# Performance work log

Hardware: AMD Instinct MI355X
Metric: run time of the kernel (lower is better)

The kernel has to match this reference:

```python
import jax, jax.numpy as jnp
import numpy as np
import math

D_MODEL = 1024
D_INNER = 2048
D_HALF = D_INNER // 2
D_STATE = 16
D_CONV = 4
DT_RANK = 64
B_SZ = 4
L = 2048


def _dw_conv(x, w, b):
    # x: (b, l, c), w: (k, 1, c) depthwise, SAME padding
    y = jax.lax.conv_general_dilated(
        x, w, window_strides=(1,), padding='SAME',
        feature_group_count=x.shape[-1],
        dimension_numbers=('NWC', 'WIO', 'NWC'))
    return y + b


def _selective_scan(u, delta, A, Bc, Cc, D):
    # u, delta: (b, l, d); Bc, Cc: (b, l, n); A: (d, n); D: (d,)
    b, l, d = u.shape
    n = A.shape[1]

    def step(h, inp):
        d_t, u_t, B_t, C_t = inp  # (b,d), (b,d), (b,n), (b,n)
        dA = jnp.exp(d_t[..., None] * A)                     # (b,d,n)
        h = dA * h + (d_t * u_t)[..., None] * B_t[:, None, :]
        y = jnp.einsum('bdn,bn->bd', h, C_t)
        return h, y

    h0 = jnp.zeros((b, d, n), u.dtype)
    xs = (jnp.moveaxis(delta, 1, 0), jnp.moveaxis(u, 1, 0),
          jnp.moveaxis(Bc, 1, 0), jnp.moveaxis(Cc, 1, 0))
    _, ys = jax.lax.scan(step, h0, xs)                       # (l,b,d)
    return jnp.moveaxis(ys, 0, 1) + u * D


def setup_inputs() -> dict:
    key = jax.random.key(0)
    ks = jax.random.split(key, 12)
    x = jax.random.normal(ks[0], (B_SZ, L, D_MODEL), jnp.float32)
    W_in = jax.random.normal(ks[1], (D_MODEL, D_INNER), jnp.float32) * (D_MODEL ** -0.5)
    conv_x_w = jax.random.normal(ks[2], (D_CONV, 1, D_HALF), jnp.float32) * (D_CONV ** -0.5)
    conv_x_b = jnp.zeros((D_HALF,), jnp.float32)
    conv_z_w = jax.random.normal(ks[3], (D_CONV, 1, D_HALF), jnp.float32) * (D_CONV ** -0.5)
    conv_z_b = jnp.zeros((D_HALF,), jnp.float32)
    W_xdbl = jax.random.normal(ks[4], (D_HALF, DT_RANK + 2 * D_STATE), jnp.float32) * (D_HALF ** -0.5)
    dt_init_std = DT_RANK ** -0.5  # dt_scale = 1.0
    W_dt = jax.random.uniform(ks[5], (DT_RANK, D_HALF), jnp.float32, -dt_init_std, dt_init_std)
    rand_vals = jax.random.uniform(ks[6], (D_HALF,))
    dt_bias = jnp.exp(rand_vals * (math.log(0.1) - math.log(0.001)) + math.log(0.001))
    dt_bias = jnp.clip(dt_bias, 1e-4)
    inv_dt = dt_bias + jnp.log(-jnp.expm1(-dt_bias))
    D = jnp.ones((D_HALF,), jnp.float32)
    W_out = jax.random.normal(ks[7], (D_INNER, D_MODEL), jnp.float32) * (D_INNER ** -0.5)
    b_out = jnp.zeros((D_MODEL,), jnp.float32)
    return dict(x=x, W_in=W_in, conv_x_w=conv_x_w, conv_x_b=conv_x_b,
                conv_z_w=conv_z_w, conv_z_b=conv_z_b, W_xdbl=W_xdbl,
                W_dt=W_dt, inv_dt=inv_dt, D=D, W_out=W_out, b_out=b_out)


def reference(x, W_in, conv_x_w, conv_x_b, conv_z_w, conv_z_b, W_xdbl,
              W_dt, inv_dt, D, W_out, b_out):
    xz = x @ W_in                                            # (b,l,d_inner), no bias
    xs, z = jnp.split(xz, 2, axis=-1)                        # (b,l,d_half) each
    # A = -exp(log(arange(1..N))) tiled over channels
    A = -jnp.tile(jnp.arange(1, D_STATE + 1, dtype=jnp.float32), (D_HALF, 1))  # (d,n)
    xs = jax.nn.silu(_dw_conv(xs, conv_x_w, conv_x_b))
    z = jax.nn.silu(_dw_conv(z, conv_z_w, conv_z_b))
    x_dbl = xs @ W_xdbl                                      # (b,l,dt_rank+2n)
    dt_low, Bc, Cc = jnp.split(x_dbl, [DT_RANK, DT_RANK + D_STATE], axis=-1)
    dt = dt_low @ W_dt + inv_dt                              # Dense with bias_init=inv_dt
    delta = jax.nn.softplus(dt + inv_dt)                     # scan adds delta_bias=inv_dt again (faithful)
    y = _selective_scan(xs, delta, A, Bc, Cc, D)             # (b,l,d_half)
    y = jnp.concatenate([y, z], axis=-1)                     # (b,l,d_inner)
    return y @ W_out + b_out
```

## Files before the change

kernel.cpp:

```cpp
#include <hip/hip_runtime.h>
#include <hip/hip_bf16.h>
#include <math.h>

#define B_SZ 4
#define LSEQ 2048
#define DM 1024
#define DI 2048
#define DH 1024
#define DS 16
#define DTR 64
#define RTOT 96
#define MROWS (B_SZ * LSEQ)

#define NCH 32
#define CHUNK 64

#define KD 192
#define KDP 200

typedef short bf8_t __attribute__((ext_vector_type(8)));
typedef float f4_t __attribute__((ext_vector_type(4)));

__device__ __forceinline__ unsigned short f2bfbits(float v) {
  __hip_bfloat16 h = __float2bfloat16(v);
  return *(unsigned short*)&h;
}
__device__ __forceinline__ float bfu_lo(unsigned int v) {
  unsigned int x = v << 16;
  return *(float*)&x;
}
__device__ __forceinline__ float bfu_hi(unsigned int v) {
  unsigned int x = v & 0xffff0000u;
  return *(float*)&x;
}
__device__ __forceinline__ float bf16f(unsigned short h) {
  unsigned int x = ((unsigned int)h) << 16;
  return *(float*)&x;
}

__device__ __forceinline__ void gl_lds16(const void* g, void* l) {
  __builtin_amdgcn_global_load_lds(
      (const __attribute__((address_space(1))) unsigned int*)g,
      (__attribute__((address_space(3))) unsigned int*)l,
      16, 0, 0);
}

__device__ __forceinline__ void ld8f(const float* p, unsigned short* d) {
  const float4 a = ((const float4*)p)[0];
  const float4 b = ((const float4*)p)[1];
  d[0] = f2bfbits(a.x); d[1] = f2bfbits(a.y); d[2] = f2bfbits(a.z); d[3] = f2bfbits(a.w);
  d[4] = f2bfbits(b.x); d[5] = f2bfbits(b.y); d[6] = f2bfbits(b.z); d[7] = f2bfbits(b.w);
}

#define VMCNT(n) asm volatile("s_waitcnt vmcnt(" #n ")" ::: "memory")
#define LGKM0 asm volatile("s_waitcnt lgkmcnt(0)" ::: "memory")

__global__ void probe_kernel(const unsigned short* __restrict__ p, int* __restrict__ flag) {
  int lane = threadIdx.x;
  int sane = 0;
#pragma unroll
  for (int j = 0; j < 4; j++) {
    unsigned short lo = p[(lane * 4 + j) * 2];
    int e = (lo >> 7) & 0xFF;
    sane += (e <= 130) ? 1 : 0;
  }
  sane += __shfl_xor(sane, 1, 64);
  sane += __shfl_xor(sane, 2, 64);
  sane += __shfl_xor(sane, 4, 64);
  sane += __shfl_xor(sane, 8, 64);
  sane += __shfl_xor(sane, 16, 64);
  sane += __shfl_xor(sane, 32, 64);
  if (lane == 0) *flag = (sane >= 220) ? 1 : 0;
}

__global__ __launch_bounds__(256) void cast_kernel(
    const int* __restrict__ flag, const float* __restrict__ x,
    unsigned short* __restrict__ xbf) {
  if (*flag == 1) return;
  int i = (blockIdx.x * 256 + threadIdx.x) * 8;
  unsigned short d[8];
  ld8f(x + i, d);
  *(uint4*)&xbf[i] = *(uint4*)d;
}

#define PREP_TOT 78848
__global__ __launch_bounds__(256) void prep_kernel(
    const int* __restrict__ flag,
    const void* s0, const void* s1, const void* s2, const void* s3,
    const void* s4, const void* s5, const void* s6, const void* s7,
    float* __restrict__ out) {
  int i = blockIdx.x * 256 + threadIdx.x;
  if (i >= PREP_TOT) return;
  const void* src; int off;
  if      (i < 4096)   { src = s0; off = i; }
  else if (i < 5120)   { src = s1; off = i - 4096; }
  else if (i < 9216)   { src = s2; off = i - 5120; }
  else if (i < 10240)  { src = s3; off = i - 9216; }
  else if (i < 75776)  { src = s4; off = i - 10240; }
  else if (i < 76800)  { src = s5; off = i - 75776; }
  else if (i < 77824)  { src = s6; off = i - 76800; }
  else                 { src = s7; off = i - 77824; }
  float v = (*flag == 1) ? __bfloat162float(((const __hip_bfloat16*)src)[off])
                         : ((const float*)src)[off];
  out[i] = v;
}

__global__ __launch_bounds__(256) void transpose_kernel(
    const int* __restrict__ flag, const void* __restrict__ W,
    unsigned short* __restrict__ Wt, int K, int N) {
  __shared__ unsigned short tile[32][33];
  int n0 = blockIdx.x * 32, k0 = blockIdx.y * 32;
  int c = threadIdx.x & 31, r8 = threadIdx.x >> 5;
  bool isbf = (*flag == 1);
#pragma unroll
  for (int p = 0; p < 4; p++) {
    int r = r8 + p * 8;
    unsigned short v;
    if (isbf) v = ((const unsigned short*)W)[(size_t)(k0 + r) * N + n0 + c];
    else      v = f2bfbits(((const float*)W)[(size_t)(k0 + r) * N + n0 + c]);
    tile[r][c] = v;
  }
  __syncthreads();
#pragma unroll
  for (int p = 0; p < 4; p++) {
    int r = r8 + p * 8;
    Wt[(size_t)(n0 + r) * K + k0 + c] = tile[c][r];
  }
}

__global__ __launch_bounds__(256) void transpose_pad_kernel(
    const int* __restrict__ flag, const void* __restrict__ W,
    unsigned short* __restrict__ Wt) {
  __shared__ unsigned short tile[32][33];
  int n0 = blockIdx.x * 32, k0 = blockIdx.y * 32;
  int c = threadIdx.x & 31, r8 = threadIdx.x >> 5;
  bool isbf = (*flag == 1);
#pragma unroll
  for (int p = 0; p < 4; p++) {
    int r = r8 + p * 8;
    unsigned short v = 0;
    if (n0 + c < RTOT) {
      if (isbf) v = ((const unsigned short*)W)[(size_t)(k0 + r) * RTOT + n0 + c];
      else      v = f2bfbits(((const float*)W)[(size_t)(k0 + r) * RTOT + n0 + c]);
    }
    tile[r][c] = v;
  }
  __syncthreads();
#pragma unroll
  for (int p = 0; p < 4; p++) {
    int r = r8 + p * 8;
    Wt[(size_t)(n0 + r) * DH + k0 + c] = tile[c][r];
  }
}

__global__ __launch_bounds__(256) void wdtt_kernel(
    const float* __restrict__ Wdt, unsigned short* __restrict__ Wdtt) {
  __shared__ unsigned short th[32][33], tl[32][33];
  int n0 = blockIdx.x * 32, k0 = blockIdx.y * 32;
  int c = threadIdx.x & 31, r8 = threadIdx.x >> 5;
#pragma unroll
  for (int p = 0; p < 4; p++) {
    int r = r8 + p * 8;
    float w = Wdt[(size_t)(k0 + r) * DH + n0 + c];
    unsigned short hi = f2bfbits(w);
    th[r][c] = hi;
    tl[r][c] = f2bfbits(w - bf16f(hi));
  }
  __syncthreads();
#pragma unroll
  for (int p = 0; p < 4; p++) {
    int r = r8 + p * 8;
    unsigned short hi = th[c][r], lo = tl[c][r];
    size_t base = (size_t)(n0 + r) * KD + k0 + c;
    Wdtt[base] = hi;
    Wdtt[base + 64] = hi;
    Wdtt[base + 128] = lo;
  }
}

template <int BN, bool OUT_BY_FLAG>
__global__ __launch_bounds__(512, 2) void gemm_bk32(
    const int* __restrict__ flag,
    const unsigned short* __restrict__ A1, const unsigned short* __restrict__ A0,
    const unsigned short* __restrict__ Bt,
    const float* __restrict__ bias, void* __restrict__ C,
    int N, int K) {
  extern __shared__ __align__(16) unsigned short lds[];
  constexpr int A_BUF = 256 * 32;
  constexpr int B_BUF = BN * 32;
  constexpr int B_OFF = 4 * A_BUF;
  constexpr int NF = BN / 64;
  constexpr int NB_LD = BN / 128;

  const int flagv = *flag;
  const unsigned short* Ap = (flagv == 1) ? A1 : A0;

  const int tid = threadIdx.x;
  const int lane = tid & 63;
  const int wave = tid >> 6;
  const int quad = lane >> 4;
  const int l16 = lane & 15;
  const int wm = wave >> 2;
  const int wn = wave & 3;

  const int NB = gridDim.x, MB = gridDim.y;
  int L = blockIdx.y * NB + blockIdx.x;
  int xcd = L & 7;
  int w = L >> 3;
  int m_band = xcd * (MB >> 3) + (w / NB);
  int n_blk = w % NB;
  const int m0 = m_band * 256;
  const int n0 = n_blk * BN;

  const int NT = K >> 5;

  f4_t acc[8][NF] = {};

  auto stage = [&](int kt) {
    const int buf = kt & 3;
    const int k0 = kt * 32;
    unsigned short* Ad = lds + buf * A_BUF;
#pragma unroll
    for (int j = 0; j < 2; j++) {
      int ch = tid + j * 512;
      int mi = ch >> 2, s = ch & 3;
      int ki = s ^ ((mi >> 1) & 3);
      gl_lds16(Ap + (size_t)(m0 + mi) * K + k0 + ki * 8,
               Ad + (j * 512 + wave * 64) * 8);
    }
    unsigned short* Bd = lds + B_OFF + buf * B_BUF;
#pragma unroll
    for (int j = 0; j < NB_LD; j++) {
      int ch = tid + j * 512;
      int ni = ch >> 2, s = ch & 3;
      int ki = s ^ ((ni >> 1) & 3);
      gl_lds16(Bt + (size_t)(n0 + ni) * K + k0 + ki * 8,
               Bd + (j * 512 + wave * 64) * 8);
    }
  };

  stage(0); stage(1); stage(2);

  for (int t = 0; t < NT; t++) {
    if (t + 2 < NT) {
      if constexpr (NF == 4) VMCNT(8); else VMCNT(6);
    } else if (t + 1 < NT) {
      if constexpr (NF == 4) VMCNT(4); else VMCNT(3);
    } else {
      VMCNT(0);
    }
    __builtin_amdgcn_s_barrier();

    const unsigned short* Ac = lds + (t & 3) * A_BUF;
    const unsigned short* Bc = lds + B_OFF + (t & 3) * B_BUF;
    bf8_t af[8], bfr[NF];
#pragma unroll
    for (int ti = 0; ti < 8; ti++) {
      int r = wm * 128 + ti * 16 + l16;
      af[ti] = *(const bf8_t*)&Ac[(r * 4 + (quad ^ ((r >> 1) & 3))) * 8];
    }
#pragma unroll
    for (int tj = 0; tj < NF; tj++) {
      int rn = wn * (BN / 4) + tj * 16 + l16;
      bfr[tj] = *(const bf8_t*)&Bc[(rn * 4 + (quad ^ ((rn >> 1) & 3))) * 8];
    }
    if (t + 3 < NT) stage(t + 3);

    LGKM0;
    __builtin_amdgcn_sched_barrier(0);
    __builtin_amdgcn_s_setprio(1);
#pragma unroll
    for (int ti = 0; ti < 8; ti++)
#pragma unroll
      for (int tj = 0; tj < NF; tj++)
        acc[ti][tj] = __builtin_amdgcn_mfma_f32_16x16x32_bf16(
            af[ti], bfr[tj], acc[ti][tj], 0, 0, 0);
    __builtin_amdgcn_s_setprio(0);
    __builtin_amdgcn_s_barrier();
  }

#pragma unroll
  for (int ti = 0; ti < 8; ti++) {
#pragma unroll
    for (int tj = 0; tj < NF; tj++) {
      int col = n0 + wn * (BN / 4) + tj * 16 + l16;
      float bv = bias ? bias[col] : 0.f;
#pragma unroll
      for (int r = 0; r < 4; r++) {
        int row = m0 + wm * 128 + ti * 16 + quad * 4 + r;
        float v = acc[ti][tj][r] + bv;
        if constexpr (!OUT_BY_FLAG) {
          __builtin_nontemporal_store(f2bfbits(v),
              (unsigned short*)C + (size_t)row * N + col);
        } else {
          if (flagv == 1)
            __builtin_nontemporal_store(f2bfbits(v),
                (unsigned short*)C + (size_t)row * N + col);
          else
            __builtin_nontemporal_store(v, (float*)C + (size_t)row * N + col);
        }
      }
    }
  }
}

__global__ __launch_bounds__(256) void xdbl_kernel(
    const unsigned short* __restrict__ A, const unsigned short* __restrict__ Bt,
    float* __restrict__ xdbl, unsigned short* __restrict__ Adelta) {
  const int tid = threadIdx.x;
  const int wave = tid >> 6;
  const int lane = tid & 63;
  const int quad = lane >> 4;
  const int l16 = lane & 15;
  const int m0 = blockIdx.x * 32 + (wave & 1) * 16;
  const int c0 = (wave >> 1) * 48;

  f4_t acc[3] = {};
  const unsigned short* Ar = A + (size_t)(m0 + l16) * DH + quad * 8;
  const unsigned short* B0 = Bt + (size_t)(c0 + l16) * DH + quad * 8;
  const unsigned short* B1 = Bt + (size_t)(c0 + 16 + l16) * DH + quad * 8;
  const unsigned short* B2 = Bt + (size_t)(c0 + 32 + l16) * DH + quad * 8;

#pragma unroll 4
  for (int k0 = 0; k0 < DH; k0 += 32) {
    bf8_t af = *(const bf8_t*)(Ar + k0);
    bf8_t b0 = *(const bf8_t*)(B0 + k0);
    bf8_t b1 = *(const bf8_t*)(B1 + k0);
    bf8_t b2 = *(const bf8_t*)(B2 + k0);
    acc[0] = __builtin_amdgcn_mfma_f32_16x16x32_bf16(af, b0, acc[0], 0, 0, 0);
    acc[1] = __builtin_amdgcn_mfma_f32_16x16x32_bf16(af, b1, acc[1], 0, 0, 0);
    acc[2] = __builtin_amdgcn_mfma_f32_16x16x32_bf16(af, b2, acc[2], 0, 0, 0);
  }

#pragma unroll
  for (int tj = 0; tj < 3; tj++) {
    int col = c0 + tj * 16 + l16;
#pragma unroll
    for (int r = 0; r < 4; r++) {
      int row = m0 + quad * 4 + r;
      float v = acc[tj][r];
      if (col < 64) {
        unsigned short hi = f2bfbits(v);
        unsigned short lo = f2bfbits(v - bf16f(hi));
        size_t base = (size_t)row * KD + col;
        Adelta[base] = hi;
        Adelta[base + 64] = lo;
        Adelta[base + 128] = hi;
      } else {
        xdbl[(size_t)row * RTOT + col] = v;
      }
    }
  }
}

__global__ __launch_bounds__(256) void delta_mfma_kernel(
    const unsigned short* __restrict__ Ad,
    const unsigned short* __restrict__ Bd,
    const float* __restrict__ inv_dt,
    const unsigned short* __restrict__ xs,
    unsigned int* __restrict__ du) {
  __shared__ __align__(16) unsigned short Bs[128 * KDP];
  const int tid = threadIdx.x;
  const int wave = tid >> 6;
  const int lane = tid & 63;
  const int quad = lane >> 4;
  const int l16 = lane & 15;
  const int m0 = blockIdx.x * 64 + wave * 16;
  const int n0 = blockIdx.y * 128;

#pragma unroll
  for (int i = 0; i < 12; i++) {
    int ch = tid + i * 256;
    int row = ch / 24, cs = ch % 24;
    uint4 v = *(const uint4*)(Bd + (size_t)(n0 + row) * KD + cs * 8);
    *(uint4*)&Bs[row * KDP + cs * 8] = v;
  }

  bf8_t a[6];
  const unsigned short* Ar = Ad + (size_t)(m0 + l16) * KD + quad * 8;
#pragma unroll
  for (int ks = 0; ks < 6; ks++) a[ks] = *(const bf8_t*)(Ar + ks * 32);

  __syncthreads();

  f4_t acc[8] = {};
#pragma unroll
  for (int ks = 0; ks < 6; ks++) {
#pragma unroll
    for (int nj = 0; nj < 8; nj++) {
      bf8_t b = *(const bf8_t*)&Bs[(nj * 16 + l16) * KDP + quad * 8 + ks * 32];
      acc[nj] = __builtin_amdgcn_mfma_f32_16x16x32_bf16(a[ks], b, acc[nj], 0, 0, 0);
    }
  }

#pragma unroll
  for (int nj = 0; nj < 8; nj++) {
    int col = n0 + nj * 16 + l16;
    float bias2 = 2.f * inv_dt[col];
#pragma unroll
    for (int r = 0; r < 4; r++) {
      int row = m0 + quad * 4 + r;
      float v = acc[nj][r] + bias2;
      float sp = (v > 0.f) ? (v + __logf(1.f + __expf(-v)))
                           : __logf(1.f + __expf(v));
      unsigned int lo = f2bfbits(sp);
      unsigned int hi = xs[(size_t)row * DH + col];
      du[(size_t)row * DH + col] = lo | (hi << 16);
    }
  }
}

__global__ __launch_bounds__(256) void conv_silu_kernel(
    const unsigned short* __restrict__ xz,
    const float* __restrict__ wx, const float* __restrict__ bx,
    const float* __restrict__ wz, const float* __restrict__ bz,
    unsigned short* __restrict__ xs_bf, unsigned short* __restrict__ cat) {
  int gid = blockIdx.x * 256 + threadIdx.x;
  int cg = gid & 127;
  int c0 = cg * 8;
  int g = gid >> 7;
  int m0 = g * 4;
  int t0 = m0 & (LSEQ - 1);
  int mbase = m0 - t0;

  float wxr[4][8], wzr[4][8];
#pragma unroll
  for (int j = 0; j < 4; j++) {
    *(float4*)&wxr[j][0] = *(const float4*)&wx[j * DH + c0];
    *(float4*)&wxr[j][4] = *(const float4*)&wx[j * DH + c0 + 4];
    *(float4*)&wzr[j][0] = *(const float4*)&wz[j * DH + c0];
    *(float4*)&wzr[j][4] = *(const float4*)&wz[j * DH + c0 + 4];
  }

  float ax[4][8], az[4][8];
#pragma unroll
  for (int o = 0; o < 4; o++)
#pragma unroll
    for (int i = 0; i < 8; i++) { ax[o][i] = bx[c0 + i]; az[o][i] = bz[c0 + i]; }

#pragma unroll
  for (int rr = 0; rr < 7; rr++) {
    int tt = t0 - 1 + rr;
    if (tt < 0 || tt >= LSEQ) continue;
    size_t row = (size_t)(mbase + tt);
    uint4 vx = *(const uint4*)&xz[row * DI + c0];
    uint4 vz = *(const uint4*)&xz[row * DI + DH + c0];
    const unsigned int* px = (const unsigned int*)&vx;
    const unsigned int* pz = (const unsigned int*)&vz;
    float xv[8], zv[8];
#pragma unroll
    for (int q = 0; q < 4; q++) {
      xv[q * 2] = bfu_lo(px[q]); xv[q * 2 + 1] = bfu_hi(px[q]);
      zv[q * 2] = bfu_lo(pz[q]); zv[q * 2 + 1] = bfu_hi(pz[q]);
    }
#pragma unroll
    for (int o = 0; o < 4; o++) {
      int j = rr - o;
      if (j < 0 || j > 3) continue;
#pragma unroll
      for (int i = 0; i < 8; i++) {
        ax[o][i] = fmaf(wxr[j][i], xv[i], ax[o][i]);
        az[o][i] = fmaf(wzr[j][i], zv[i], az[o][i]);
      }
    }
  }

#pragma unroll
  for (int o = 0; o < 4; o++) {
    unsigned short sx[8], sz[8];
#pragma unroll
    for (int i = 0; i < 8; i++) {
      float vx = ax[o][i] / (1.f + __expf(-ax[o][i]));
      float vz = az[o][i] / (1.f + __expf(-az[o][i]));
      sx[i] = f2bfbits(vx);
      sz[i] = f2bfbits(vz);
    }
    size_t m = (size_t)(m0 + o);
    *(uint4*)&xs_bf[m * DH + c0] = *(uint4*)sx;
    *(uint4*)&cat[m * DI + DH + c0] = *(uint4*)sz;
  }
}

__global__ __launch_bounds__(256) void scan_pass1(
    const unsigned int* __restrict__ du, const float* __restrict__ xdbl,
    float* __restrict__ Echunks, float* __restrict__ hp) {
  const int tid = threadIdx.x;
  const int d = blockIdx.x * 256 + tid;
  const int c = blockIdx.y, b = blockIdx.z;
  const int row0 = b * LSEQ + c * CHUNK;
  __shared__ float sBC[CHUNK][32];
#pragma unroll
  for (int i = 0; i < 2; i++) {
    int task = tid + i * 256;
    int r = task >> 3, seg = task & 7;
    *(float4*)&sBC[r][seg * 4] =
        *(const float4*)&xdbl[(size_t)(row0 + r) * RTOT + DTR + seg * 4];
  }
  __syncthreads();
  float h[16];
#pragma unroll
  for (int n = 0; n < 16; n++) h[n] = 0.f;
  float E = 1.f;
  for (int t = 0; t < CHUNK; t++) {
    unsigned int v = du[(size_t)(row0 + t) * DH + d];
    float dt = bfu_lo(v), ut = bfu_hi(v);
    float e = __expf(-dt);
    E *= e;
    float dv = dt * ut;
    float p = 1.f;
#pragma unroll
    for (int n = 0; n < 16; n++) {
      p *= e;
      h[n] = fmaf(p, h[n], dv * sBC[t][n]);
    }
  }
  Echunks[((size_t)c * B_SZ + b) * DH + d] = E;
#pragma unroll
  for (int n = 0; n < 16; n++)
    hp[(((size_t)c * B_SZ + b) * 16 + n) * DH + d] = h[n];
}

__global__ __launch_bounds__(256) void scan_pass2(
    const float* __restrict__ Echunks, const float* __restrict__ hp,
    float* __restrict__ hs) {
  int t = blockIdx.x * 256 + threadIdx.x;
  int d = t & 1023;
  int n = (t >> 10) & 15;
  int b = t >> 14;
  float h = 0.f;
  const int k0 = n + 1;
  for (int c = 0; c < NCH; c++) {
    float E = Echunks[((size_t)c * B_SZ + b) * DH + d];
    float a = 1.f, base = E;
    int k = k0;
#pragma unroll
    for (int i = 0; i < 5; i++) {
      if (k & 1) a *= base;
      base *= base;
      k >>= 1;
    }
    size_t idx = (((size_t)c * B_SZ + b) * 16 + n) * DH + d;
    hs[idx] = h;
    h = fmaf(a, h, hp[idx]);
  }
}

__global__ __launch_bounds__(256) void scan_pass3(
    const unsigned int* __restrict__ du, const float* __restrict__ xdbl,
    const float* __restrict__ hs, const float* __restrict__ Dvec,
    __hip_bfloat16* __restrict__ cat) {
  const int tid = threadIdx.x;
  const int d = blockIdx.x * 256 + tid;
  const int c = blockIdx.y, b = blockIdx.z;
  const int row0 = b * LSEQ + c * CHUNK;
  __shared__ float sBC[CHUNK][32];
#pragma unroll
  for (int i = 0; i < 2; i++) {
    int task = tid + i * 256;
    int r = task >> 3, seg = task & 7;
    *(float4*)&sBC[r][seg * 4] =
        *(const float4*)&xdbl[(size_t)(row0 + r) * RTOT + DTR + seg * 4];
  }
  __syncthreads();
  float h[16];
#pragma unroll
  for (int n = 0; n < 16; n++)
    h[n] = hs[(((size_t)c * B_SZ + b) * 16 + n) * DH + d];
  const float Dd = Dvec[d];
  for (int t = 0; t < CHUNK; t++) {
    unsigned int v = du[(size_t)(row0 + t) * DH + d];
    float dt = bfu_lo(v), ut = bfu_hi(v);
    float e = __expf(-dt);
    float dv = dt * ut;
    float p = 1.f, y = 0.f;
#pragma unroll
    for (int n = 0; n < 16; n++) {
      p *= e;
      h[n] = fmaf(p, h[n], dv * sBC[t][n]);
      y = fmaf(h[n], sBC[t][16 + n], y);
    }
    y = fmaf(ut, Dd, y);
    cat[(size_t)(row0 + t) * DI + d] = __float2bfloat16(y);
  }
}

extern "C" void kernel_launch(void* const* d_in, const int* in_sizes, int n_in,
                              void* d_out, int out_size, void* d_ws, size_t ws_size,
                              hipStream_t stream) {
  char* ws = (char*)d_ws;
  __hip_bfloat16* xz  = (__hip_bfloat16*)(ws);
  unsigned int* du    = (unsigned int*)(ws);
  __hip_bfloat16* xs  = (__hip_bfloat16*)(ws + ((size_t)32 << 20));
  unsigned short* xbf = (unsigned short*)(ws + ((size_t)48 << 20));
  __hip_bfloat16* cat = (__hip_bfloat16*)(ws + ((size_t)64 << 20));
  float* xdbl         = (float*)(ws + ((size_t)96 << 20));
  float* Echunks      = (float*)(ws + ((size_t)99 << 20));
  float* hp           = (float*)(ws + ((size_t)100 << 20));
  unsigned short* Wdtt = (unsigned short*)(ws + ((size_t)100 << 20));
  float* hs           = (float*)(ws + ((size_t)108 << 20));
  unsigned short* Adelta = (unsigned short*)(ws + ((size_t)108 << 20));
  unsigned short* Wt_in  = (unsigned short*)(ws + ((size_t)116 << 20));
  unsigned short* Wt_out = (unsigned short*)(ws + ((size_t)120 << 20));
  unsigned short* Wxt    = (unsigned short*)(ws + ((size_t)124 << 20));
  float* cw           = (float*)(ws + ((size_t)125 << 20));
  int* flag           = (int*)(ws + ((size_t)126 << 20));

  const float* conv_xwf = cw + 0;
  const float* conv_xbf = cw + 4096;
  const float* conv_zwf = cw + 5120;
  const float* conv_zbf = cw + 9216;
  const float* Wdtf     = cw + 10240;
  const float* inv_dtf  = cw + 75776;
  const float* Df       = cw + 76800;
  const float* b_outf   = cw + 77824;

  (void)hipFuncSetAttribute(reinterpret_cast<const void*>(&gemm_bk32<256, false>),
                            hipFuncAttributeMaxDynamicSharedMemorySize, 131072);
  (void)hipFuncSetAttribute(reinterpret_cast<const void*>(&gemm_bk32<128, true>),
                            hipFuncAttributeMaxDynamicSharedMemorySize, 98304);

  probe_kernel<<<1, 64, 0, stream>>>((const unsigned short*)d_in[0], flag);
  cast_kernel<<<4096, 256, 0, stream>>>(flag, (const float*)d_in[0], xbf);
  prep_kernel<<<(PREP_TOT + 255) / 256, 256, 0, stream>>>(
      flag, d_in[2], d_in[3], d_in[4], d_in[5], d_in[7], d_in[8], d_in[9],
      d_in[11], cw);
  transpose_kernel<<<dim3(DI / 32, DM / 32), 256, 0, stream>>>(
      flag, d_in[1], Wt_in, DM, DI);
  transpose_kernel<<<dim3(DM / 32, DI / 32), 256, 0, stream>>>(
      flag, d_in[10], Wt_out, DI, DM);
  transpose_pad_kernel<<<dim3(4, DH / 32), 256, 0, stream>>>(flag, d_in[6], Wxt);
  wdtt_kernel<<<dim3(DH / 32, 2), 256, 0, stream>>>(Wdtf, Wdtt);

  gemm_bk32<256, false><<<dim3(DI / 256, MROWS / 256), 512, 131072, stream>>>(
      flag, (const unsigned short*)d_in[0], xbf, Wt_in,
      (const float*)nullptr, xz, DI, DM);
  conv_silu_kernel<<<(MROWS / 4) * 128 / 256, 256, 0, stream>>>(
      (const unsigned short*)xz, conv_xwf, conv_xbf, conv_zwf, conv_zbf,
      (unsigned short*)xs, (unsigned short*)cat);
  xdbl_kernel<<<MROWS / 32, 256, 0, stream>>>(
      (const unsigned short*)xs, Wxt, xdbl, Adelta);
  delta_mfma_kernel<<<dim3(MROWS / 64, DH / 128), 256, 0, stream>>>(
      Adelta, Wdtt, inv_dtf, (const unsigned short*)xs, du);
  scan_pass1<<<dim3(4, NCH, B_SZ), 256, 0, stream>>>(du, xdbl, Echunks, hp);
  scan_pass2<<<256, 256, 0, stream>>>(Echunks, hp, hs);
  scan_pass3<<<dim3(4, NCH, B_SZ), 256, 0, stream>>>(du, xdbl, hs, Df, cat);
  gemm_bk32<128, true><<<dim3(DM / 128, MROWS / 256), 512, 98304, stream>>>(
      flag, (const unsigned short*)cat, (const unsigned short*)cat, Wt_out,
      b_outf, d_out, DM, DI);
}
```

Before: 360.1 us.

## Prefetch scan chunk inputs into LDS and break power-chain dependency in scan passes

The scan pass1 and pass3 kernels now load the whole 64-row chunk of packed delta/u values into LDS up front with direct global-to-LDS loads, so the per-timestep loop no longer issues dependent global loads. The serial chain of multiplies that computed exp(-dt)^n is replaced by a shallow power ladder, and pass3 splits the C-dot accumulation into four partial sums to shorten the dependency chain. This raises LDS use to 72 KB per block, which lowers occupancy, and the power ladder may round slightly differently.

```diff
diff --git a/kernel.cpp b/kernel.cpp
--- a/kernel.cpp
+++ b/kernel.cpp
@@ -50,6 +50,15 @@
   const float4 b = ((const float4*)p)[1];
   d[0] = f2bfbits(a.x); d[1] = f2bfbits(a.y); d[2] = f2bfbits(a.z); d[3] = f2bfbits(a.w);
   d[4] = f2bfbits(b.x); d[5] = f2bfbits(b.y); d[6] = f2bfbits(b.z); d[7] = f2bfbits(b.w);
+}
+
+__device__ __forceinline__ void pow_ladder(float e, float* pw) {
+  float e2 = e * e, e4 = e2 * e2, e8 = e4 * e4;
+  float e3 = e2 * e, e5 = e4 * e, e6 = e4 * e2, e7 = e4 * e3;
+  pw[0] = e;        pw[1] = e2;       pw[2] = e3;       pw[3] = e4;
+  pw[4] = e5;       pw[5] = e6;       pw[6] = e7;       pw[7] = e8;
+  pw[8] = e8 * e;   pw[9] = e8 * e2;  pw[10] = e8 * e3; pw[11] = e8 * e4;
+  pw[12] = e8 * e5; pw[13] = e8 * e6; pw[14] = e8 * e7; pw[15] = e8 * e8;
 }
 
 #define VMCNT(n) asm volatile("s_waitcnt vmcnt(" #n ")" ::: "memory")
@@ -484,36 +493,48 @@
 __global__ __launch_bounds__(256) void scan_pass1(
     const unsigned int* __restrict__ du, const float* __restrict__ xdbl,
     float* __restrict__ Echunks, float* __restrict__ hp) {
+  extern __shared__ __align__(16) unsigned int sm1[];
+  unsigned int* sDU = sm1;
+  float* sBC = (float*)(sm1 + CHUNK * 256);
   const int tid = threadIdx.x;
-  const int d = blockIdx.x * 256 + tid;
+  const int wave = tid >> 6;
+  const int d0 = blockIdx.x * 256;
   const int c = blockIdx.y, b = blockIdx.z;
   const int row0 = b * LSEQ + c * CHUNK;
-  __shared__ float sBC[CHUNK][32];
+
+  const unsigned int* src = du + (size_t)row0 * DH + d0;
+#pragma unroll
+  for (int i = 0; i < 16; i++) {
+    int ch = tid + i * 256;
+    int r = ch >> 6, cs = ch & 63;
+    gl_lds16(src + (size_t)r * DH + cs * 4, sDU + (i * 256 + wave * 64) * 4);
+  }
 #pragma unroll
   for (int i = 0; i < 2; i++) {
     int task = tid + i * 256;
     int r = task >> 3, seg = task & 7;
-    *(float4*)&sBC[r][seg * 4] =
+    *(float4*)&sBC[r * 32 + seg * 4] =
         *(const float4*)&xdbl[(size_t)(row0 + r) * RTOT + DTR + seg * 4];
   }
   __syncthreads();
+
   float h[16];
 #pragma unroll
   for (int n = 0; n < 16; n++) h[n] = 0.f;
   float E = 1.f;
   for (int t = 0; t < CHUNK; t++) {
-    unsigned int v = du[(size_t)(row0 + t) * DH + d];
+    unsigned int v = sDU[t * 256 + tid];
     float dt = bfu_lo(v), ut = bfu_hi(v);
     float e = __expf(-dt);
     E *= e;
     float dv = dt * ut;
-    float p = 1.f;
-#pragma unroll
-    for (int n = 0; n < 16; n++) {
-      p *= e;
-      h[n] = fmaf(p, h[n], dv * sBC[t][n]);
-    }
-  }
+    float pw[16];
+    pow_ladder(e, pw);
+#pragma unroll
+    for (int n = 0; n < 16; n++)
+      h[n] = fmaf(pw[n], h[n], dv * sBC[t * 32 + n]);
+  }
+  const int d = d0 + tid;
   Echunks[((size_t)c * B_SZ + b) * DH + d] = E;
 #pragma unroll
   for (int n = 0; n < 16; n++)
@@ -549,36 +570,58 @@
     const unsigned int* __restrict__ du, const float* __restrict__ xdbl,
     const float* __restrict__ hs, const float* __restrict__ Dvec,
     __hip_bfloat16* __restrict__ cat) {
+  extern __shared__ __align__(16) unsigned int sm1[];
+  unsigned int* sDU = sm1;
+  float* sBC = (float*)(sm1 + CHUNK * 256);
   const int tid = threadIdx.x;
-  const int d = blockIdx.x * 256 + tid;
+  const int wave = tid >> 6;
+  const int d0 = blockIdx.x * 256;
   const int c = blockIdx.y, b = blockIdx.z;
   const int row0 = b * LSEQ + c * CHUNK;
-  __shared__ float sBC[CHUNK][32];
+
+  const unsigned int* src = du + (size_t)row0 * DH + d0;
+#pragma unroll
+  for (int i = 0; i < 16; i++) {
+    int ch = tid + i * 256;
+    int r = ch >> 6, cs = ch & 63;
+    gl_lds16(src + (size_t)r * DH + cs * 4, sDU + (i * 256 + wave * 64) * 4);
+  }
 #pragma unroll
   for (int i = 0; i < 2; i++) {
     int task = tid + i * 256;
     int r = task >> 3, seg = task & 7;
-    *(float4*)&sBC[r][seg * 4] =
+    *(float4*)&sBC[r * 32 + seg * 4] =
         *(const float4*)&xdbl[(size_t)(row0 + r) * RTOT + DTR + seg * 4];
   }
-  __syncthreads();
+
+  const int d = d0 + tid;
   float h[16];
 #pragma unroll
   for (int n = 0; n < 16; n++)
     h[n] = hs[(((size_t)c * B_SZ + b) * 16 + n) * DH + d];
   const float Dd = Dvec[d];
+  __syncthreads();
+
   for (int t = 0; t < CHUNK; t++) {
-    unsigned int v = du[(size_t)(row0 + t) * DH + d];
+    unsigned int v = sDU[t * 256 + tid];
     float dt = bfu_lo(v), ut = bfu_hi(v);
     float e = __expf(-dt);
     float dv = dt * ut;
-    float p = 1.f, y = 0.f;
-#pragma unroll
-    for (int n = 0; n < 16; n++) {
-      p *= e;
-      h[n] = fmaf(p, h[n], dv * sBC[t][n]);
-      y = fmaf(h[n], sBC[t][16 + n], y);
-    }
+    float pw[16];
+    pow_ladder(e, pw);
+    float y0 = 0.f, y1 = 0.f, y2 = 0.f, y3 = 0.f;
+#pragma unroll
+    for (int n = 0; n < 16; n += 4) {
+      h[n]     = fmaf(pw[n],     h[n],     dv * sBC[t * 32 + n]);
+      h[n + 1] = fmaf(pw[n + 1], h[n + 1], dv * sBC[t * 32 + n + 1]);
+      h[n + 2] = fmaf(pw[n + 2], h[n + 2], dv * sBC[t * 32 + n + 2]);
+      h[n + 3] = fmaf(pw[n + 3], h[n + 3], dv * sBC[t * 32 + n + 3]);
+      y0 = fmaf(h[n],     sBC[t * 32 + 16 + n],     y0);
+      y1 = fmaf(h[n + 1], sBC[t * 32 + 16 + n + 1], y1);
+      y2 = fmaf(h[n + 2], sBC[t * 32 + 16 + n + 2], y2);
+      y3 = fmaf(h[n + 3], sBC[t * 32 + 16 + n + 3], y3);
+    }
+    float y = (y0 + y1) + (y2 + y3);
     y = fmaf(ut, Dd, y);
     cat[(size_t)(row0 + t) * DI + d] = __float2bfloat16(y);
   }
@@ -618,6 +661,10 @@
                             hipFuncAttributeMaxDynamicSharedMemorySize, 131072);
   (void)hipFuncSetAttribute(reinterpret_cast<const void*>(&gemm_bk32<128, true>),
                             hipFuncAttributeMaxDynamicSharedMemorySize, 98304);
+  (void)hipFuncSetAttribute(reinterpret_cast<const void*>(&scan_pass1),
+                            hipFuncAttributeMaxDynamicSharedMemorySize, 73728);
+  (void)hipFuncSetAttribute(reinterpret_cast<const void*>(&scan_pass3),
+                            hipFuncAttributeMaxDynamicSharedMemorySize, 73728);
 
   probe_kernel<<<1, 64, 0, stream>>>((const unsigned short*)d_in[0], flag);
   cast_kernel<<<4096, 256, 0, stream>>>(flag, (const float*)d_in[0], xbf);
@@ -641,9 +688,9 @@
       (const unsigned short*)xs, Wxt, xdbl, Adelta);
   delta_mfma_kernel<<<dim3(MROWS / 64, DH / 128), 256, 0, stream>>>(
       Adelta, Wdtt, inv_dtf, (const unsigned short*)xs, du);
-  scan_pass1<<<dim3(4, NCH, B_SZ), 256, 0, stream>>>(du, xdbl, Echunks, hp);
+  scan_pass1<<<dim3(4, NCH, B_SZ), 256, 73728, stream>>>(du, xdbl, Echunks, hp);
   scan_pass2<<<256, 256, 0, stream>>>(Echunks, hp, hs);
-  scan_pass3<<<dim3(4, NCH, B_SZ), 256, 0, stream>>>(du, xdbl, hs, Df, cat);
+  scan_pass3<<<dim3(4, NCH, B_SZ), 256, 73728, stream>>>(du, xdbl, hs, Df, cat);
   gemm_bk32<128, true><<<dim3(DM / 128, MROWS / 256), 512, 98304, stream>>>(
       flag, (const unsigned short*)cat, (const unsigned short*)cat, Wt_out,
       b_outf, d_out, DM, DI);
```

Measured after the change: 344.4 us. -4.4%, faster.
